# Kernel tuning notes

Measured on AMD Instinct MI355X. Metric: run time of the kernel, lower is better.

Reference implementation:

```python
import jax, jax.numpy as jnp
import numpy as np

E = 1408      # hidden_size
H = 16        # num heads
D = E // H    # head_dim = 88
S = 1025      # (448/14)^2 + 1 cls token
B = 8


def setup_inputs() -> dict:
    key = jax.random.key(0)
    ks = jax.random.split(key, 11)
    scale = 1.0 / np.sqrt(E)
    inp = {
        "hidden_states": jax.random.normal(ks[0], (B, S, E), dtype=jnp.float32),
    }
    # rotary freqs as cos/sin of random angles, shape (S, D//2)
    theta = jax.random.uniform(ks[1], (S, D // 2), dtype=jnp.float32) * (2.0 * np.pi)
    inp["freqs_cos"] = jnp.cos(theta)
    inp["freqs_sin"] = jnp.sin(theta)
    # projection weights stored torch-style: (out_features, in_features)
    inp["q_w"] = jax.random.normal(ks[2], (E, E), dtype=jnp.float32) * scale
    inp["q_b"] = jax.random.normal(ks[3], (E,), dtype=jnp.float32) * scale
    inp["k_w"] = jax.random.normal(ks[4], (E, E), dtype=jnp.float32) * scale
    inp["k_b"] = jax.random.normal(ks[5], (E,), dtype=jnp.float32) * scale
    inp["v_w"] = jax.random.normal(ks[6], (E, E), dtype=jnp.float32) * scale
    inp["v_b"] = jax.random.normal(ks[7], (E,), dtype=jnp.float32) * scale
    inp["o_w"] = jax.random.normal(ks[8], (E, E), dtype=jnp.float32) * scale
    inp["o_b"] = jax.random.normal(ks[9], (E,), dtype=jnp.float32) * scale
    return inp


def _apply_rope(x, cos, sin):
    # x: (B, S, H, D); interpret last dim as D//2 complex pairs (re, im)
    xr = x.astype(jnp.float32).reshape(*x.shape[:-1], D // 2, 2)
    re, im = xr[..., 0], xr[..., 1]
    c = cos[None, :, None, :]  # broadcast over batch and heads
    s = sin[None, :, None, :]
    out_re = re * c - im * s
    out_im = re * s + im * c
    return jnp.stack([out_re, out_im], axis=-1).reshape(x.shape).astype(x.dtype)


def reference(hidden_states, freqs_cos, freqs_sin, q_w, q_b, k_w, k_b, v_w, v_b, o_w, o_b):
    b, s, _ = hidden_states.shape
    q = (hidden_states @ q_w.T + q_b).reshape(b, s, H, D)
    k = (hidden_states @ k_w.T + k_b).reshape(b, s, H, D)
    v = (hidden_states @ v_w.T + v_b).reshape(b, s, H, D)
    q = _apply_rope(q, freqs_cos, freqs_sin)
    k = _apply_rope(k, freqs_cos, freqs_sin)
    # (B, H, S, D)
    q = q.transpose(0, 2, 1, 3)
    k = k.transpose(0, 2, 1, 3)
    v = v.transpose(0, 2, 1, 3)
    scores = jnp.einsum('bhqd,bhkd->bhqk', q, k) / np.sqrt(D)
    attn = jax.nn.softmax(scores.astype(jnp.float32), axis=-1).astype(q.dtype)
    out = jnp.einsum('bhqk,bhkd->bqhd', attn, v).reshape(b, s, H * D)
    out = out @ o_w.T + o_b
    return out, attn
```

## Files before the change

kernel.cpp:

```cpp
#include <hip/hip_runtime.h>

typedef unsigned short u16;
typedef __attribute__((ext_vector_type(8))) short short8;
typedef __attribute__((ext_vector_type(4))) float f32x4;

#define E_DIM 1408
#define H_HEADS 16
#define D_HEAD 88
#define S_SEQ 1025
#define B_BATCH 8
#define S_PAD 1088
#define D_PAD 128
#define M_ROWS 8200
#define M_PAD 8320

__device__ __forceinline__ u16 f2bf(float f){
  union { float f; unsigned u; } x; x.f = f;
  unsigned r = x.u + 0x7fffu + ((x.u >> 16) & 1u);
  return (u16)(r >> 16);
}

__device__ __forceinline__ void gload16(const void* g, void* l){
  __builtin_amdgcn_global_load_lds(
      (const __attribute__((address_space(1))) void*)g,
      (__attribute__((address_space(3))) void*)l, 16, 0, 0);
}

__device__ __forceinline__ f32x4 mfma16(short8 a, short8 b, f32x4 c){
  return __builtin_amdgcn_mfma_f32_16x16x32_bf16(a, b, c, 0, 0, 0);
}

__global__ __launch_bounds__(256) void cvt_kernel(const float* __restrict__ src,
                                                  u16* __restrict__ dst, int n8){
  int i = blockIdx.x * 256 + threadIdx.x;
  if (i >= n8) return;
  const float4* s4 = (const float4*)src;
  float4 a = s4[2*i], b = s4[2*i+1];
  union { u16 u[8]; short8 v; } o;
  o.u[0]=f2bf(a.x); o.u[1]=f2bf(a.y); o.u[2]=f2bf(a.z); o.u[3]=f2bf(a.w);
  o.u[4]=f2bf(b.x); o.u[5]=f2bf(b.y); o.u[6]=f2bf(b.z); o.u[7]=f2bf(b.w);
  ((short8*)dst)[i] = o.v;
}

__global__ __launch_bounds__(256) void zero_pads_kernel(u16* __restrict__ Q,
                                                        u16* __restrict__ K,
                                                        u16* __restrict__ Vt){
  int i = blockIdx.x * 256 + threadIdx.x;
  const int n1 = 128 * S_PAD * 8;
  const int n2 = 128 * 96 * 63;
  if (i < n1){
    int d = 88 + (i & 7); int t = i >> 3;
    int s = t % S_PAD; int bh = t / S_PAD;
    size_t o = ((size_t)bh * S_PAD + s) * D_PAD + d;
    Q[o] = 0; K[o] = 0;
  } else if (i < n1 + n2){
    int j = i - n1;
    int d = j % 96; int t = j / 96;
    int sp = 1025 + t % 63; int bh = t / 63;
    Vt[((size_t)bh * D_PAD + d) * S_PAD + sp] = 0;
  }
}

template<int EPI>
__global__ __launch_bounds__(256) void gemm_bt(
    const u16* __restrict__ A, const u16* __restrict__ W,
    const float* __restrict__ bias,
    u16* __restrict__ outB, float* __restrict__ outF,
    const float* __restrict__ fcos, const float* __restrict__ fsin)
{
  __shared__ u16 As[128*32];
  __shared__ u16 Bs[128*32];
  const int tid = threadIdx.x;
  const int lane = tid & 63, wid = tid >> 6;
  const int cl = lane & 15, grp = lane >> 4;
  const int n0 = blockIdx.x * 128, m0 = blockIdx.y * 128;
  const int wm = (wid >> 1) * 64, wn = (wid & 1) * 64;
  f32x4 acc[4][4] = {};

  for (int k0 = 0; k0 < E_DIM; k0 += 32){
    __syncthreads();
#pragma unroll
    for (int rd = 0; rd < 2; ++rd){
      int G = rd * 256 + tid;
      int row = G >> 2, cg = G & 3;
      gload16(A + (size_t)(m0 + row) * E_DIM + k0 + cg * 8, (char*)As + (size_t)G * 16);
      gload16(W + (size_t)(n0 + row) * E_DIM + k0 + cg * 8, (char*)Bs + (size_t)G * 16);
    }
    __syncthreads();
    short8 av[4], bv[4];
#pragma unroll
    for (int i = 0; i < 4; ++i) av[i] = *(const short8*)&As[(wm + i*16 + cl)*32 + grp*8];
#pragma unroll
    for (int j = 0; j < 4; ++j) bv[j] = *(const short8*)&Bs[(wn + j*16 + cl)*32 + grp*8];
#pragma unroll
    for (int i = 0; i < 4; ++i)
#pragma unroll
      for (int j = 0; j < 4; ++j)
        acc[i][j] = mfma16(av[i], bv[j], acc[i][j]);
  }

#pragma unroll
  for (int i = 0; i < 4; ++i){
#pragma unroll
    for (int j = 0; j < 4; ++j){
      const int jcol = n0 + wn + j*16 + cl;
      const float bsv = bias[jcol];
      const int hh = jcol / 88;
      const int dd = jcol - hh * 88;
#pragma unroll
      for (int r = 0; r < 4; ++r){
        const int rrow = m0 + wm + i*16 + grp*4 + r;
        float v = acc[i][j][r] + bsv;
        if (EPI == 0 || EPI == 1){
          float other = __shfl_xor(v, 1);
          int bb = rrow / 1025;
          int spos = rrow - bb * 1025;
          int pp = dd >> 1;
          float c = fcos[spos * 44 + pp];
          float s = fsin[spos * 44 + pp];
          float o = fmaf(v, c, (jcol & 1) ? (other * s) : -(other * s));
          if (rrow < M_ROWS){
            size_t dst = (((size_t)(bb * 16 + hh)) * S_PAD + spos) * D_PAD + dd;
            outB[dst] = f2bf(o);
          }
        } else if (EPI == 2){
          if (rrow < M_ROWS){
            int bb = rrow / 1025;
            int spos = rrow - bb * 1025;
            size_t dst = (((size_t)(bb * 16 + hh)) * D_PAD + dd) * S_PAD + spos;
            outB[dst] = f2bf(v);
          }
        } else {
          if (rrow < M_ROWS) outF[(size_t)rrow * E_DIM + jcol] = v;
        }
      }
    }
  }
}

__global__ __launch_bounds__(256) void attn_kernel(
    const u16* __restrict__ Qb, const u16* __restrict__ Kb,
    const u16* __restrict__ Vtb, float* __restrict__ attn,
    u16* __restrict__ AO)
{
  __shared__ u16 Ks[64 * 128];
  __shared__ u16 Vs[96 * 64];
  __shared__ u16 Ps[4][16 * 72];
  const int tid = threadIdx.x, wid = tid >> 6, lane = tid & 63;
  const int cl = lane & 15, grp = lane >> 4;
  const int qt = blockIdx.x, bh = blockIdx.y;
  const int b = bh >> 4, h = bh & 15;
  const u16* Qg = Qb + (size_t)bh * S_PAD * D_PAD;
  const u16* Kg = Kb + (size_t)bh * S_PAD * D_PAD;
  const u16* Vg = Vtb + (size_t)bh * D_PAD * S_PAD;
  const int qbase = qt * 64 + wid * 16;
  const float scale = 0.10660035817780521f;

  short8 qf[3];
#pragma unroll
  for (int s = 0; s < 3; ++s)
    qf[s] = *(const short8*)&Qg[(size_t)(qbase + cl) * D_PAD + s * 32 + grp * 8];

  float m_run = -1e30f, l_run = 0.f;

  for (int kt = 0; kt < 17; ++kt){
    __syncthreads();
#pragma unroll
    for (int rd = 0; rd < 4; ++rd){
      int G = rd * 256 + tid;
      int row = G >> 4, c = G & 15;
      gload16(Kg + (size_t)(kt * 64 + row) * D_PAD + ((c ^ (row & 15)) * 8),
              (char*)Ks + (size_t)G * 16);
    }
    __syncthreads();
#pragma unroll
    for (int ks = 0; ks < 4; ++ks){
      f32x4 sc = {0.f, 0.f, 0.f, 0.f};
#pragma unroll
      for (int s = 0; s < 3; ++s){
        int row = ks * 16 + cl;
        short8 kf = *(const short8*)&Ks[row * 128 + (((s * 4 + grp) ^ (row & 15)) * 8)];
        sc = mfma16(kf, qf[s], sc);
      }
      int kbase = kt * 64 + ks * 16 + grp * 4;
      float x0 = (kbase + 0 < 1025) ? sc[0] * scale : -1e30f;
      float x1 = (kbase + 1 < 1025) ? sc[1] * scale : -1e30f;
      float x2 = (kbase + 2 < 1025) ? sc[2] * scale : -1e30f;
      float x3 = (kbase + 3 < 1025) ? sc[3] * scale : -1e30f;
      float lm = fmaxf(fmaxf(x0, x1), fmaxf(x2, x3));
      float mn = fmaxf(m_run, lm);
      l_run = l_run * __expf(m_run - mn)
            + __expf(x0 - mn) + __expf(x1 - mn) + __expf(x2 - mn) + __expf(x3 - mn);
      m_run = mn;
    }
  }
#pragma unroll
  for (int off = 16; off < 64; off <<= 1){
    float mo = __shfl_xor(m_run, off);
    float lo = __shfl_xor(l_run, off);
    float mn = fmaxf(m_run, mo);
    l_run = l_run * __expf(m_run - mn) + lo * __expf(mo - mn);
    m_run = mn;
  }
  float linv = 1.0f / l_run;

  f32x4 oacc[6] = {};

  for (int kt = 0; kt < 17; ++kt){
    __syncthreads();
#pragma unroll
    for (int rd = 0; rd < 4; ++rd){
      int G = rd * 256 + tid;
      int row = G >> 4, c = G & 15;
      gload16(Kg + (size_t)(kt * 64 + row) * D_PAD + ((c ^ (row & 15)) * 8),
              (char*)Ks + (size_t)G * 16);
    }
#pragma unroll
    for (int rd = 0; rd < 3; ++rd){
      int G = rd * 256 + tid;
      int row = G >> 3, c = G & 7;
      gload16(Vg + (size_t)row * S_PAD + kt * 64 + ((c ^ (row & 7)) * 8),
              (char*)Vs + (size_t)G * 16);
    }
    __syncthreads();
#pragma unroll
    for (int ks = 0; ks < 4; ++ks){
      f32x4 sc = {0.f, 0.f, 0.f, 0.f};
#pragma unroll
      for (int s = 0; s < 3; ++s){
        int row = ks * 16 + cl;
        short8 kf = *(const short8*)&Ks[row * 128 + (((s * 4 + grp) ^ (row & 15)) * 8)];
        sc = mfma16(kf, qf[s], sc);
      }
      int kbase = kt * 64 + ks * 16 + grp * 4;
      float p0 = (kbase + 0 < 1025) ? __expf(sc[0] * scale - m_run) * linv : 0.f;
      float p1 = (kbase + 1 < 1025) ? __expf(sc[1] * scale - m_run) * linv : 0.f;
      float p2 = (kbase + 2 < 1025) ? __expf(sc[2] * scale - m_run) * linv : 0.f;
      float p3 = (kbase + 3 < 1025) ? __expf(sc[3] * scale - m_run) * linv : 0.f;
      int qrow = qbase + cl;
      if (qrow < 1025){
        size_t ab = ((size_t)bh * 1025 + qrow) * 1025 + kbase;
        if (kbase + 3 < 1025){
          attn[ab] = p0; attn[ab+1] = p1; attn[ab+2] = p2; attn[ab+3] = p3;
        } else {
          if (kbase     < 1025) attn[ab]   = p0;
          if (kbase + 1 < 1025) attn[ab+1] = p1;
          if (kbase + 2 < 1025) attn[ab+2] = p2;
        }
      }
      unsigned long long pk = (unsigned long long)f2bf(p0)
                            | ((unsigned long long)f2bf(p1) << 16)
                            | ((unsigned long long)f2bf(p2) << 32)
                            | ((unsigned long long)f2bf(p3) << 48);
      *(unsigned long long*)&Ps[wid][cl * 72 + ks * 16 + grp * 4] = pk;
    }
#pragma unroll
    for (int kc = 0; kc < 2; ++kc){
      short8 pf = *(const short8*)&Ps[wid][cl * 72 + kc * 32 + grp * 8];
#pragma unroll
      for (int dt = 0; dt < 6; ++dt){
        int row = dt * 16 + cl;
        short8 vf = *(const short8*)&Vs[row * 64 + ((((kc * 4) + grp) ^ (row & 7)) * 8)];
        oacc[dt] = mfma16(pf, vf, oacc[dt]);
      }
    }
  }

#pragma unroll
  for (int dt = 0; dt < 6; ++dt){
    int d = dt * 16 + cl;
    if (d < 88){
#pragma unroll
      for (int r = 0; r < 4; ++r){
        int qrow = qbase + grp * 4 + r;
        if (qrow < 1025)
          AO[((size_t)b * 1025 + qrow) * E_DIM + h * 88 + d] = f2bf(oacc[dt][r]);
      }
    }
  }
}

extern "C" void kernel_launch(void* const* d_in, const int* in_sizes, int n_in,
                              void* d_out, int out_size, void* d_ws, size_t ws_size,
                              hipStream_t stream)
{
  const float* hs   = (const float*)d_in[0];
  const float* fcos = (const float*)d_in[1];
  const float* fsin = (const float*)d_in[2];
  const float* q_w  = (const float*)d_in[3];
  const float* q_b  = (const float*)d_in[4];
  const float* k_w  = (const float*)d_in[5];
  const float* k_b  = (const float*)d_in[6];
  const float* v_w  = (const float*)d_in[7];
  const float* v_b  = (const float*)d_in[8];
  const float* o_w  = (const float*)d_in[9];
  const float* o_b  = (const float*)d_in[10];
  float* out0 = (float*)d_out;
  float* attn = out0 + (size_t)B_BATCH * S_SEQ * E_DIM;

  char* ws = (char*)d_ws;
  size_t off = 0;
  auto take = [&](size_t bytes){
    char* p = ws + off; off += (bytes + 255) & ~(size_t)255; return p;
  };
  u16* Xb  = (u16*)take((size_t)M_PAD * E_DIM * 2);
  u16* Wb  = (u16*)take((size_t)4 * E_DIM * E_DIM * 2);
  u16* Qb  = (u16*)take((size_t)128 * S_PAD * D_PAD * 2);
  u16* Kb  = (u16*)take((size_t)128 * S_PAD * D_PAD * 2);
  u16* Vtb = (u16*)take((size_t)128 * D_PAD * S_PAD * 2);
  u16* AO  = (u16*)take((size_t)M_PAD * E_DIM * 2);

  cvt_kernel<<<(1443200 + 255) / 256, 256, 0, stream>>>(hs, Xb, 1443200);
  cvt_kernel<<<968, 256, 0, stream>>>(q_w, Wb + 0 * (size_t)E_DIM * E_DIM, 247808);
  cvt_kernel<<<968, 256, 0, stream>>>(k_w, Wb + 1 * (size_t)E_DIM * E_DIM, 247808);
  cvt_kernel<<<968, 256, 0, stream>>>(v_w, Wb + 2 * (size_t)E_DIM * E_DIM, 247808);
  cvt_kernel<<<968, 256, 0, stream>>>(o_w, Wb + 3 * (size_t)E_DIM * E_DIM, 247808);
  zero_pads_kernel<<<7376, 256, 0, stream>>>(Qb, Kb, Vtb);

  dim3 gg(11, 65);
  gemm_bt<0><<<gg, 256, 0, stream>>>(Xb, Wb + 0 * (size_t)E_DIM * E_DIM, q_b, Qb,  nullptr, fcos, fsin);
  gemm_bt<1><<<gg, 256, 0, stream>>>(Xb, Wb + 1 * (size_t)E_DIM * E_DIM, k_b, Kb,  nullptr, fcos, fsin);
  gemm_bt<2><<<gg, 256, 0, stream>>>(Xb, Wb + 2 * (size_t)E_DIM * E_DIM, v_b, Vtb, nullptr, fcos, fsin);

  attn_kernel<<<dim3(17, 128), 256, 0, stream>>>(Qb, Kb, Vtb, attn, AO);

  gemm_bt<3><<<gg, 256, 0, stream>>>(AO, Wb + 3 * (size_t)E_DIM * E_DIM, o_b, nullptr, out0, fcos, fsin);
}
```

Measured before the change: 591.9 us.

## Fuse QKV projections into one GEMM and restructure attention with 32x32 MFMA and double buffering

```diff
diff --git a/kernel.cpp b/kernel.cpp
--- a/kernel.cpp
+++ b/kernel.cpp
@@ -3,10 +3,10 @@
 typedef unsigned short u16;
 typedef __attribute__((ext_vector_type(8))) short short8;
 typedef __attribute__((ext_vector_type(4))) float f32x4;
+typedef __attribute__((ext_vector_type(16))) float f32x16;
 
 #define E_DIM 1408
 #define H_HEADS 16
-#define D_HEAD 88
 #define S_SEQ 1025
 #define B_BATCH 8
 #define S_PAD 1088
@@ -14,6 +14,8 @@
 #define M_ROWS 8200
 #define M_PAD 8320
 
+struct __attribute__((packed, aligned(4))) f4u { float x, y, z, w; };
+
 __device__ __forceinline__ u16 f2bf(float f){
   union { float f; unsigned u; } x; x.f = f;
   unsigned r = x.u + 0x7fffu + ((x.u >> 16) & 1u);
@@ -28,6 +30,9 @@
 
 __device__ __forceinline__ f32x4 mfma16(short8 a, short8 b, f32x4 c){
   return __builtin_amdgcn_mfma_f32_16x16x32_bf16(a, b, c, 0, 0, 0);
+}
+__device__ __forceinline__ f32x16 mfma32(short8 a, short8 b, f32x16 c){
+  return __builtin_amdgcn_mfma_f32_32x32x16_bf16(a, b, c, 0, 0, 0);
 }
 
 __global__ __launch_bounds__(256) void cvt_kernel(const float* __restrict__ src,
@@ -47,7 +52,8 @@
                                                         u16* __restrict__ Vt){
   int i = blockIdx.x * 256 + threadIdx.x;
   const int n1 = 128 * S_PAD * 8;
-  const int n2 = 128 * 96 * 63;
+  const int n2 = 128 * 63 * 96;
+  const int n3 = 128 * 96 * 63;
   if (i < n1){
     int d = 88 + (i & 7); int t = i >> 3;
     int s = t % S_PAD; int bh = t / S_PAD;
@@ -56,16 +62,24 @@
   } else if (i < n1 + n2){
     int j = i - n1;
     int d = j % 96; int t = j / 96;
+    int s = 1025 + t % 63; int bh = t / 63;
+    size_t o = ((size_t)bh * S_PAD + s) * D_PAD + d;
+    Q[o] = 0; K[o] = 0;
+  } else if (i < n1 + n2 + n3){
+    int j = i - n1 - n2;
+    int d = j % 96; int t = j / 96;
     int sp = 1025 + t % 63; int bh = t / 63;
     Vt[((size_t)bh * D_PAD + d) * S_PAD + sp] = 0;
   }
 }
 
-template<int EPI>
+template<int MODE>
 __global__ __launch_bounds__(256) void gemm_bt(
     const u16* __restrict__ A, const u16* __restrict__ W,
-    const float* __restrict__ bias,
-    u16* __restrict__ outB, float* __restrict__ outF,
+    const float* __restrict__ b_q, const float* __restrict__ b_k,
+    const float* __restrict__ b_v,
+    u16* __restrict__ Qb, u16* __restrict__ Kb, u16* __restrict__ Vtb,
+    float* __restrict__ outF,
     const float* __restrict__ fcos, const float* __restrict__ fsin)
 {
   __shared__ u16 As[128*32];
@@ -74,6 +88,7 @@
   const int lane = tid & 63, wid = tid >> 6;
   const int cl = lane & 15, grp = lane >> 4;
   const int n0 = blockIdx.x * 128, m0 = blockIdx.y * 128;
+  const int region = (MODE == 0) ? (blockIdx.x / 11) : 0;
   const int wm = (wid >> 1) * 64, wn = (wid & 1) * 64;
   f32x4 acc[4][4] = {};
 
@@ -99,36 +114,39 @@
         acc[i][j] = mfma16(av[i], bv[j], acc[i][j]);
   }
 
+  const float* bias = (MODE == 1) ? b_q : (region == 0 ? b_q : (region == 1 ? b_k : b_v));
+
 #pragma unroll
   for (int i = 0; i < 4; ++i){
 #pragma unroll
     for (int j = 0; j < 4; ++j){
       const int jcol = n0 + wn + j*16 + cl;
-      const float bsv = bias[jcol];
-      const int hh = jcol / 88;
-      const int dd = jcol - hh * 88;
+      const int jl = jcol - region * E_DIM;
+      const float bsv = bias[jl];
+      const int hh = jl / 88;
+      const int dd = jl - hh * 88;
 #pragma unroll
       for (int r = 0; r < 4; ++r){
         const int rrow = m0 + wm + i*16 + grp*4 + r;
         float v = acc[i][j][r] + bsv;
-        if (EPI == 0 || EPI == 1){
+        if (MODE == 0 && region <= 1){
           float other = __shfl_xor(v, 1);
           int bb = rrow / 1025;
           int spos = rrow - bb * 1025;
           int pp = dd >> 1;
           float c = fcos[spos * 44 + pp];
           float s = fsin[spos * 44 + pp];
-          float o = fmaf(v, c, (jcol & 1) ? (other * s) : -(other * s));
+          float o = fmaf(v, c, (jl & 1) ? (other * s) : -(other * s));
           if (rrow < M_ROWS){
             size_t dst = (((size_t)(bb * 16 + hh)) * S_PAD + spos) * D_PAD + dd;
-            outB[dst] = f2bf(o);
+            (region ? Kb : Qb)[dst] = f2bf(o);
           }
-        } else if (EPI == 2){
+        } else if (MODE == 0){
           if (rrow < M_ROWS){
             int bb = rrow / 1025;
             int spos = rrow - bb * 1025;
             size_t dst = (((size_t)(bb * 16 + hh)) * D_PAD + dd) * S_PAD + spos;
-            outB[dst] = f2bf(v);
+            Vtb[dst] = f2bf(v);
           }
         } else {
           if (rrow < M_ROWS) outF[(size_t)rrow * E_DIM + jcol] = v;
@@ -138,143 +156,163 @@
   }
 }
 
-__global__ __launch_bounds__(256) void attn_kernel(
+#define STAGE_K(buf, kt)                                                        \
+  {                                                                             \
+    _Pragma("unroll")                                                           \
+    for (int rd = 0; rd < 2; ++rd){                                             \
+      int G = rd * 512 + tid;                                                   \
+      int row = G >> 4, c = G & 15;                                             \
+      gload16(Kg + (size_t)((kt) * 64 + row) * 128 + ((c ^ (row & 15)) * 8),    \
+              (char*)&Ks[buf][0] + (size_t)G * 16);                             \
+    }                                                                           \
+  }
+
+#define STAGE_V(buf, kt)                                                        \
+  {                                                                             \
+    { int G = tid; int row = G >> 3, c = G & 7;                                 \
+      gload16(Vg + (size_t)row * S_PAD + (kt) * 64 + ((c ^ (row & 7)) * 8),     \
+              (char*)&Vs[buf][0] + (size_t)G * 16); }                           \
+    if (tid < 256){                                                             \
+      int G = 512 + tid; int row = G >> 3, c = G & 7;                           \
+      gload16(Vg + (size_t)row * S_PAD + (kt) * 64 + ((c ^ (row & 7)) * 8),     \
+              (char*)&Vs[buf][0] + (size_t)G * 16); }                           \
+  }
+
+__global__ __launch_bounds__(512) void attn_kernel(
     const u16* __restrict__ Qb, const u16* __restrict__ Kb,
     const u16* __restrict__ Vtb, float* __restrict__ attn,
     u16* __restrict__ AO)
 {
-  __shared__ u16 Ks[64 * 128];
-  __shared__ u16 Vs[96 * 64];
-  __shared__ u16 Ps[4][16 * 72];
+  __shared__ u16 Ks[2][64 * 128];
+  __shared__ u16 Vs[2][96 * 64];
   const int tid = threadIdx.x, wid = tid >> 6, lane = tid & 63;
-  const int cl = lane & 15, grp = lane >> 4;
-  const int qt = blockIdx.x, bh = blockIdx.y;
+  const int q5 = lane & 31, hi = lane >> 5;
+  int lin = blockIdx.x + gridDim.x * blockIdx.y;
+  lin = (lin & 7) * 80 + (lin >> 3);
+  const int qt = lin % 5, bh = lin / 5;
   const int b = bh >> 4, h = bh & 15;
-  const u16* Qg = Qb + (size_t)bh * S_PAD * D_PAD;
-  const u16* Kg = Kb + (size_t)bh * S_PAD * D_PAD;
-  const u16* Vg = Vtb + (size_t)bh * D_PAD * S_PAD;
-  const int qbase = qt * 64 + wid * 16;
-  const float scale = 0.10660035817780521f;
-
-  short8 qf[3];
-#pragma unroll
-  for (int s = 0; s < 3; ++s)
-    qf[s] = *(const short8*)&Qg[(size_t)(qbase + cl) * D_PAD + s * 32 + grp * 8];
-
-  float m_run = -1e30f, l_run = 0.f;
-
+  const u16* __restrict__ Qg = Qb + (size_t)bh * S_PAD * 128;
+  const u16* __restrict__ Kg = Kb + (size_t)bh * S_PAD * 128;
+  const u16* __restrict__ Vg = Vtb + (size_t)bh * 128 * S_PAD;
+  const int qrow = qt * 256 + wid * 32 + q5;
+  const int qrowc = (qrow < S_PAD) ? qrow : (S_PAD - 1);
+  const float SCALE = 0.10660035817780521f;
+
+  short8 qf[6];
+#pragma unroll
+  for (int ds = 0; ds < 6; ++ds)
+    qf[ds] = *(const short8*)&Qg[(size_t)qrowc * 128 + ds * 16 + hi * 8];
+
+  float l_run = 0.f;
+  STAGE_K(0, 0);
+  __syncthreads();
   for (int kt = 0; kt < 17; ++kt){
+    const int cur = kt & 1;
+    if (kt < 16) STAGE_K(cur ^ 1, kt + 1);
+#pragma unroll
+    for (int ks = 0; ks < 2; ++ks){
+      f32x16 sc = {};
+      const int krow = ks * 32 + q5;
+#pragma unroll
+      for (int ds = 0; ds < 6; ++ds){
+        int c = ds * 2 + hi;
+        short8 kf = *(const short8*)&Ks[cur][krow * 128 + ((c ^ (krow & 15)) * 8)];
+        sc = mfma32(kf, qf[ds], sc);
+      }
+      if (kt == 16){
+#pragma unroll
+        for (int r = 0; r < 16; ++r){
+          int kabs = 1024 + ks * 32 + (r & 3) + 8 * (r >> 2) + 4 * hi;
+          l_run += (kabs < 1025) ? __expf(sc[r] * SCALE) : 0.f;
+        }
+      } else {
+#pragma unroll
+        for (int r = 0; r < 16; ++r) l_run += __expf(sc[r] * SCALE);
+      }
+    }
     __syncthreads();
-#pragma unroll
-    for (int rd = 0; rd < 4; ++rd){
-      int G = rd * 256 + tid;
-      int row = G >> 4, c = G & 15;
-      gload16(Kg + (size_t)(kt * 64 + row) * D_PAD + ((c ^ (row & 15)) * 8),
-              (char*)Ks + (size_t)G * 16);
+  }
+  l_run += __shfl_xor(l_run, 32);
+  const float linv = 1.0f / l_run;
+
+  f32x16 oacc[3] = {};
+  STAGE_K(0, 0);
+  STAGE_V(0, 0);
+  __syncthreads();
+  for (int kt = 0; kt < 17; ++kt){
+    const int cur = kt & 1;
+    if (kt < 16){ STAGE_K(cur ^ 1, kt + 1); STAGE_V(cur ^ 1, kt + 1); }
+#pragma unroll
+    for (int ks = 0; ks < 2; ++ks){
+      f32x16 sc = {};
+      const int krow = ks * 32 + q5;
+#pragma unroll
+      for (int ds = 0; ds < 6; ++ds){
+        int c = ds * 2 + hi;
+        short8 kf = *(const short8*)&Ks[cur][krow * 128 + ((c ^ (krow & 15)) * 8)];
+        sc = mfma32(kf, qf[ds], sc);
+      }
+#pragma unroll
+      for (int r = 0; r < 16; ++r) sc[r] = __expf(sc[r] * SCALE) * linv;
+
+      if (qrow < 1025){
+        if (kt < 16){
+          float* arow = attn + ((size_t)bh * 1025 + qrow) * 1025 + kt * 64 + ks * 32 + 4 * hi;
+#pragma unroll
+          for (int g = 0; g < 4; ++g){
+            f4u w4 = { sc[4*g], sc[4*g+1], sc[4*g+2], sc[4*g+3] };
+            *(f4u*)(arow + 8 * g) = w4;
+          }
+        } else {
+#pragma unroll
+          for (int r = 0; r < 16; ++r){
+            int kabs = 1024 + ks * 32 + (r & 3) + 8 * (r >> 2) + 4 * hi;
+            if (kabs < 1025)
+              attn[((size_t)bh * 1025 + qrow) * 1025 + kabs] = sc[r];
+          }
+        }
+      }
+
+      unsigned w[8], sx[8];
+#pragma unroll
+      for (int j = 0; j < 8; ++j)
+        w[j] = (unsigned)f2bf(sc[2*j]) | ((unsigned)f2bf(sc[2*j+1]) << 16);
+#pragma unroll
+      for (int j = 0; j < 8; ++j) sx[j] = __shfl_xor(w[j], 32);
+      union U { unsigned u[4]; short8 s8; } a0, a1;
+      a0.u[0] = hi ? sx[2] : w[0];
+      a0.u[1] = hi ? sx[3] : w[1];
+      a0.u[2] = hi ? w[2]  : sx[0];
+      a0.u[3] = hi ? w[3]  : sx[1];
+      a1.u[0] = hi ? sx[6] : w[4];
+      a1.u[1] = hi ? sx[7] : w[5];
+      a1.u[2] = hi ? w[6]  : sx[4];
+      a1.u[3] = hi ? w[7]  : sx[5];
+
+#pragma unroll
+      for (int dt = 0; dt < 3; ++dt){
+        const int vrow = dt * 32 + q5;
+        int c0 = ks * 4 + hi;
+        short8 vf0 = *(const short8*)&Vs[cur][vrow * 64 + ((c0 ^ (vrow & 7)) * 8)];
+        oacc[dt] = mfma32(a0.s8, vf0, oacc[dt]);
+        int c1 = ks * 4 + 2 + hi;
+        short8 vf1 = *(const short8*)&Vs[cur][vrow * 64 + ((c1 ^ (vrow & 7)) * 8)];
+        oacc[dt] = mfma32(a1.s8, vf1, oacc[dt]);
+      }
     }
     __syncthreads();
-#pragma unroll
-    for (int ks = 0; ks < 4; ++ks){
-      f32x4 sc = {0.f, 0.f, 0.f, 0.f};
-#pragma unroll
-      for (int s = 0; s < 3; ++s){
-        int row = ks * 16 + cl;
-        short8 kf = *(const short8*)&Ks[row * 128 + (((s * 4 + grp) ^ (row & 15)) * 8)];
-        sc = mfma16(kf, qf[s], sc);
-      }
-      int kbase = kt * 64 + ks * 16 + grp * 4;
-      float x0 = (kbase + 0 < 1025) ? sc[0] * scale : -1e30f;
-      float x1 = (kbase + 1 < 1025) ? sc[1] * scale : -1e30f;
-      float x2 = (kbase + 2 < 1025) ? sc[2] * scale : -1e30f;
-      float x3 = (kbase + 3 < 1025) ? sc[3] * scale : -1e30f;
-      float lm = fmaxf(fmaxf(x0, x1), fmaxf(x2, x3));
-      float mn = fmaxf(m_run, lm);
-      l_run = l_run * __expf(m_run - mn)
-            + __expf(x0 - mn) + __expf(x1 - mn) + __expf(x2 - mn) + __expf(x3 - mn);
-      m_run = mn;
-    }
-  }
-#pragma unroll
-  for (int off = 16; off < 64; off <<= 1){
-    float mo = __shfl_xor(m_run, off);
-    float lo = __shfl_xor(l_run, off);
-    float mn = fmaxf(m_run, mo);
-    l_run = l_run * __expf(m_run - mn) + lo * __expf(mo - mn);
-    m_run = mn;
-  }
-  float linv = 1.0f / l_run;
-
-  f32x4 oacc[6] = {};
-
-  for (int kt = 0; kt < 17; ++kt){
-    __syncthreads();
-#pragma unroll
-    for (int rd = 0; rd < 4; ++rd){
-      int G = rd * 256 + tid;
-      int row = G >> 4, c = G & 15;
-      gload16(Kg + (size_t)(kt * 64 + row) * D_PAD + ((c ^ (row & 15)) * 8),
-              (char*)Ks + (size_t)G * 16);
-    }
-#pragma unroll
-    for (int rd = 0; rd < 3; ++rd){
-      int G = rd * 256 + tid;
-      int row = G >> 3, c = G & 7;
-      gload16(Vg + (size_t)row * S_PAD + kt * 64 + ((c ^ (row & 7)) * 8),
-              (char*)Vs + (size_t)G * 16);
-    }
-    __syncthreads();
-#pragma unroll
-    for (int ks = 0; ks < 4; ++ks){
-      f32x4 sc = {0.f, 0.f, 0.f, 0.f};
-#pragma unroll
-      for (int s = 0; s < 3; ++s){
-        int row = ks * 16 + cl;
-        short8 kf = *(const short8*)&Ks[row * 128 + (((s * 4 + grp) ^ (row & 15)) * 8)];
-        sc = mfma16(kf, qf[s], sc);
-      }
-      int kbase = kt * 64 + ks * 16 + grp * 4;
-      float p0 = (kbase + 0 < 1025) ? __expf(sc[0] * scale - m_run) * linv : 0.f;
-      float p1 = (kbase + 1 < 1025) ? __expf(sc[1] * scale - m_run) * linv : 0.f;
-      float p2 = (kbase + 2 < 1025) ? __expf(sc[2] * scale - m_run) * linv : 0.f;
-      float p3 = (kbase + 3 < 1025) ? __expf(sc[3] * scale - m_run) * linv : 0.f;
-      int qrow = qbase + cl;
-      if (qrow < 1025){
-        size_t ab = ((size_t)bh * 1025 + qrow) * 1025 + kbase;
-        if (kbase + 3 < 1025){
-          attn[ab] = p0; attn[ab+1] = p1; attn[ab+2] = p2; attn[ab+3] = p3;
-        } else {
-          if (kbase     < 1025) attn[ab]   = p0;
-          if (kbase + 1 < 1025) attn[ab+1] = p1;
-          if (kbase + 2 < 1025) attn[ab+2] = p2;
-        }
-      }
-      unsigned long long pk = (unsigned long long)f2bf(p0)
-                            | ((unsigned long long)f2bf(p1) << 16)
-                            | ((unsigned long long)f2bf(p2) << 32)
-                            | ((unsigned long long)f2bf(p3) << 48);
-      *(unsigned long long*)&Ps[wid][cl * 72 + ks * 16 + grp * 4] = pk;
-    }
-#pragma unroll
-    for (int kc = 0; kc < 2; ++kc){
-      short8 pf = *(const short8*)&Ps[wid][cl * 72 + kc * 32 + grp * 8];
-#pragma unroll
-      for (int dt = 0; dt < 6; ++dt){
-        int row = dt * 16 + cl;
-        short8 vf = *(const short8*)&Vs[row * 64 + ((((kc * 4) + grp) ^ (row & 7)) * 8)];
-        oacc[dt] = mfma16(pf, vf, oacc[dt]);
-      }
-    }
-  }
-
-#pragma unroll
-  for (int dt = 0; dt < 6; ++dt){
-    int d = dt * 16 + cl;
+  }
+
+  const int qb0 = qt * 256 + wid * 32;
+#pragma unroll
+  for (int dt = 0; dt < 3; ++dt){
+    const int d = dt * 32 + q5;
     if (d < 88){
 #pragma unroll
-      for (int r = 0; r < 4; ++r){
-        int qrow = qbase + grp * 4 + r;
-        if (qrow < 1025)
-          AO[((size_t)b * 1025 + qrow) * E_DIM + h * 88 + d] = f2bf(oacc[dt][r]);
+      for (int r = 0; r < 16; ++r){
+        int qq = qb0 + (r & 3) + 8 * (r >> 2) + 4 * hi;
+        if (qq < 1025)
+          AO[((size_t)b * 1025 + qq) * E_DIM + h * 88 + d] = f2bf(oacc[dt][r]);
       }
     }
   }
@@ -315,14 +353,14 @@
   cvt_kernel<<<968, 256, 0, stream>>>(k_w, Wb + 1 * (size_t)E_DIM * E_DIM, 247808);
   cvt_kernel<<<968, 256, 0, stream>>>(v_w, Wb + 2 * (size_t)E_DIM * E_DIM, 247808);
   cvt_kernel<<<968, 256, 0, stream>>>(o_w, Wb + 3 * (size_t)E_DIM * E_DIM, 247808);
-  zero_pads_kernel<<<7376, 256, 0, stream>>>(Qb, Kb, Vtb);
-
-  dim3 gg(11, 65);
-  gemm_bt<0><<<gg, 256, 0, stream>>>(Xb, Wb + 0 * (size_t)E_DIM * E_DIM, q_b, Qb,  nullptr, fcos, fsin);
-  gemm_bt<1><<<gg, 256, 0, stream>>>(Xb, Wb + 1 * (size_t)E_DIM * E_DIM, k_b, Kb,  nullptr, fcos, fsin);
-  gemm_bt<2><<<gg, 256, 0, stream>>>(Xb, Wb + 2 * (size_t)E_DIM * E_DIM, v_b, Vtb, nullptr, fcos, fsin);
-
-  attn_kernel<<<dim3(17, 128), 256, 0, stream>>>(Qb, Kb, Vtb, attn, AO);
-
-  gemm_bt<3><<<gg, 256, 0, stream>>>(AO, Wb + 3 * (size_t)E_DIM * E_DIM, o_b, nullptr, out0, fcos, fsin);
-}
+  zero_pads_kernel<<<10400, 256, 0, stream>>>(Qb, Kb, Vtb);
+
+  gemm_bt<0><<<dim3(33, 65), 256, 0, stream>>>(Xb, Wb, q_b, k_b, v_b,
+                                               Qb, Kb, Vtb, nullptr, fcos, fsin);
+
+  attn_kernel<<<dim3(5, 128), 512, 0, stream>>>(Qb, Kb, Vtb, attn, AO);
+
+  gemm_bt<1><<<dim3(11, 65), 256, 0, stream>>>(AO, Wb + 3 * (size_t)E_DIM * E_DIM,
+                                               o_b, o_b, o_b,
+                                               nullptr, nullptr, nullptr, out0, fcos, fsin);
+}
```

After: 587.2 us. No clear change (-0.8%).
